# Performance work log

Hardware: AMD Instinct MI355X
Metric: run time of the kernel (lower is better)

The kernel has to match this reference:

```python
import jax, jax.numpy as jnp
import numpy as np

NUM_CAPS = 2          # NUM_CLASSES
R = 16 * 10 * 10 * 10 # num_route_nodes = 16000
NUM_ITERS = 3


def conv3d(x, w, b, stride):
    y = jax.lax.conv_general_dilated(
        x, w, window_strides=(stride, stride, stride), padding='VALID',
        dimension_numbers=('NCDHW', 'OIDHW', 'NCDHW'))
    return y + b[None, :, None, None, None]


def squash(t, axis=-1):
    n = jnp.linalg.norm(t, axis=axis, keepdims=True)
    scale = n ** 2 / (1 + n ** 2) / (n + 1e-8)
    return scale * t


def setup_inputs() -> dict:
    key = jax.random.key(0)
    ks = jax.random.split(key, 16)
    inp = {
        'x': jax.random.normal(ks[0], (16, 1, 29, 29, 29), jnp.float32),
        'conv1_w': 0.05 * jax.random.normal(ks[1], (128, 1, 3, 3, 3), jnp.float32),
        'conv1_b': jnp.zeros((128,), jnp.float32),
        # 8 primary capsules, each Conv3d(128,16,k=9,s=2), stacked cap-major
        'pcaps_w': 0.01 * jax.random.normal(ks[2], (8 * 16, 128, 9, 9, 9), jnp.float32),
        'pcaps_b': jnp.zeros((8 * 16,), jnp.float32),
        'route_w': 0.01 * jax.random.normal(ks[3], (NUM_CAPS, R, 8, 16), jnp.float32),
        'dec_w1': 0.05 * jax.random.normal(ks[4], (32, 512), jnp.float32),
        'dec_b1': jnp.zeros((512,), jnp.float32),
        'dec_w2': 0.05 * jax.random.normal(ks[5], (512, 2048), jnp.float32),
        'dec_b2': jnp.zeros((2048,), jnp.float32),
        'dec_w3': 0.02 * jax.random.normal(ks[6], (2048, 10240), jnp.float32),
        'dec_b3': jnp.zeros((10240,), jnp.float32),
        'dec_w4': 0.02 * jax.random.normal(ks[7], (10240, 27000), jnp.float32),
        'dec_b4': jnp.zeros((27000,), jnp.float32),
    }
    return inp


def reference(x, conv1_w, conv1_b, pcaps_w, pcaps_b, route_w,
              dec_w1, dec_b1, dec_w2, dec_b2, dec_w3, dec_b3, dec_w4, dec_b4):
    B = x.shape[0]
    # stem conv + relu: [B,128,27,27,27]
    h = jax.nn.relu(conv3d(x, conv1_w, conv1_b, 1))
    # primary capsules (8 convs fused into one): [B,128,10,10,10]
    p = conv3d(h, pcaps_w, pcaps_b, 2)
    # torch: per-capsule view(B,-1,1) then cat dim=-1 -> [B,16000,8]
    p = p.reshape(B, 8, R).transpose(0, 2, 1)
    u = squash(p, axis=-1)  # [B,R,8]

    # priors: x[:,None,:,None,:] @ W[None] -> [B,C,R,16] (singleton dim dropped)
    priors = jnp.einsum('bri,crio->bcro', u, route_w)
    priors_d = jax.lax.stop_gradient(priors)
    # torch logits have trailing dim 16 but are constant along it (delta is
    # broadcast), so [B,C,R,1] is mathematically identical.
    logits = jnp.zeros((B, NUM_CAPS, R, 1), priors.dtype)

    for i in range(NUM_ITERS):
        probs = jax.nn.softmax(logits, axis=1)  # over capsule axis
        if i == NUM_ITERS - 1:
            v = squash((probs * priors).sum(axis=2, keepdims=True))
        else:
            v = squash((probs * priors_d).sum(axis=2, keepdims=True))
            logits = logits + (priors_d * v).sum(axis=-1, keepdims=True)

    caps = v[:, :, 0, :]  # [B,C,16] (squeeze)
    classes = jnp.linalg.norm(caps, axis=-1)  # [B,C]

    # y=None branch: one-hot of argmax
    y = jax.nn.one_hot(jnp.argmax(classes, axis=1), NUM_CAPS, dtype=caps.dtype)
    d = (caps * y[:, :, None]).reshape(B, -1)  # [B,32]
    d = jax.nn.relu(d @ dec_w1 + dec_b1)
    d = jax.nn.relu(d @ dec_w2 + dec_b2)
    d = jax.nn.relu(d @ dec_w3 + dec_b3)
    recon = jax.nn.sigmoid(d @ dec_w4 + dec_b4)  # [B,27000]
    return classes, recon
```

## Files before the change

kernel.cpp:

```cpp
#include <hip/hip_runtime.h>
#include <hip/hip_bf16.h>

#define NB   16
#define C1   128
#define XS   29
#define HS   27
#define HSP  19683
#define PS   10
#define PSP  1000
#define RR   16000
#define NCAP 2
#define KTAP 729
#define HTOT 40310784L
#define SPTOT 314928

#define OFF_WT   0UL
#define OFF_H    11943936UL
#define OFF_P    52254720UL
#define OFF_U    54302720UL
#define OFF_PRI  56350720UL
#define OFF_LOG  64542720UL
#define OFF_S    65054720UL
#define OFF_V    65055232UL
#define OFF_D0   65055744UL
#define OFF_D1   65056256UL
#define OFF_D2   65064448UL
#define OFF_D3   65097216UL
#define OFF_D4   65261056UL
#define OFF_PP   65693056UL
#define OFF_D3P  82077056UL
#define OFF_D4P  84698496UL

typedef __attribute__((ext_vector_type(8))) short bf16x8;
typedef __attribute__((ext_vector_type(4))) float f32x4;

#define GL2LDS16(g, l) __builtin_amdgcn_global_load_lds( \
    (const __attribute__((address_space(1))) void*)(g), \
    (__attribute__((address_space(3))) void*)(l), 16, 0, 0)

__global__ void prep_w2(const float* __restrict__ w, __hip_bfloat16* __restrict__ w2) {
    __shared__ float tile[32][33];
    int tap0 = blockIdx.x * 32;
    int ic0  = blockIdx.y * 32;
    int oc   = blockIdx.z;
    int tx = threadIdx.x & 31, ty = threadIdx.x >> 5;
    #pragma unroll
    for (int j = 0; j < 32; j += 8) {
        int tap = tap0 + tx, ic = ic0 + ty + j;
        if (tap < KTAP) tile[ty + j][tx] = w[(size_t)oc * 93312 + (size_t)ic * KTAP + tap];
    }
    __syncthreads();
    #pragma unroll
    for (int j = 0; j < 32; j += 8) {
        int tap = tap0 + ty + j, ic = ic0 + tx;
        if (tap < KTAP)
            w2[((size_t)tap * 128 + oc) * 128 + ic] = __float2bfloat16(tile[tx][ty + j]);
    }
}

__global__ __launch_bounds__(256) void conv1_relu(const float* __restrict__ x,
                                                  const float* __restrict__ w,
                                                  const float* __restrict__ bias,
                                                  __hip_bfloat16* __restrict__ h) {
    int t = threadIdx.x;
    int c = t & 127;
    float wr[27];
    #pragma unroll
    for (int k = 0; k < 27; k++) wr[k] = w[c * 27 + k];
    float bv = bias[c];
    int sp_base = blockIdx.x * 32 + (t >> 7);
    #pragma unroll 4
    for (int i = 0; i < 16; i++) {
        int spg = sp_base + i * 2;
        if (spg >= SPTOT) return;
        int b = spg / HSP, sp = spg % HSP;
        int z = sp / 729, y = (sp / 27) % 27, xx = sp % 27;
        const float* xb = x + (size_t)b * (XS * XS * XS) + ((size_t)z * XS + y) * XS + xx;
        float xv[27];
        #pragma unroll
        for (int dz = 0; dz < 3; dz++)
            #pragma unroll
            for (int dy = 0; dy < 3; dy++)
                #pragma unroll
                for (int dx = 0; dx < 3; dx++)
                    xv[(dz * 3 + dy) * 3 + dx] = xb[((size_t)dz * XS + dy) * XS + dx];
        float acc = bv;
        #pragma unroll
        for (int k = 0; k < 27; k++) acc = fmaf(xv[k], wr[k], acc);
        h[(size_t)spg * 128 + c] = __float2bfloat16(fmaxf(acc, 0.f));
    }
}

__global__ __launch_bounds__(512, 2) void pcaps_mfma(const ushort* __restrict__ hu,
                                                     const ushort* __restrict__ wu,
                                                     float* __restrict__ pp) {
    __shared__ __align__(16) ushort As[2 * 256 * 32];
    __shared__ __align__(16) ushort Bs[2 * 128 * 32];
    int t = threadIdx.x;
    int bid = blockIdx.x;
    int g = bid & 7;
    int m0 = (bid >> 3) * 256;
    int tap_begin = g * 92;
    int tap_end   = min(KTAP, tap_begin + 92);
    int KP = (tap_end - tap_begin) * 4;

    int a_base[2], a_seg[2];
    #pragma unroll
    for (int q = 0; q < 2; q++) {
        int idx = q * 512 + t;
        int row = idx >> 2;
        int m = m0 + row; if (m > 15999) m = 15999;
        int b = m / PSP, sp = m % PSP;
        int oz = sp / 100, oy = (sp / 10) % 10, ox = sp % 10;
        a_base[q] = (((b * HS + 2 * oz) * HS + 2 * oy) * HS + 2 * ox) * 128;
        a_seg[q]  = (((idx & 3) ^ ((idx >> 3) & 3))) * 8;
    }
    int b_base = (t >> 2) * 128;
    int b_seg  = (((t & 3) ^ ((t >> 3) & 3))) * 8;

    int lane = t & 63, wave = t >> 6;
    int wr = wave >> 1, wc = wave & 1;
    int l15 = lane & 15, kq = lane >> 4;
    int slot8 = (kq ^ ((l15 >> 1) & 3)) * 8;

    f32x4 acc[4][4];
    #pragma unroll
    for (int i = 0; i < 4; i++)
        #pragma unroll
        for (int j = 0; j < 4; j++) acc[i][j] = (f32x4)0.f;

#define STAGE(KPI, NB_)  {                                                   \
        int tap_ = tap_begin + ((KPI) >> 2), ich_ = ((KPI) & 3) * 32;        \
        int dz_ = tap_ / 81, dy_ = (tap_ / 9) % 9, dx_ = tap_ % 9;           \
        int toff_ = ((dz_ * HS + dy_) * HS + dx_) * 128 + ich_;              \
        const ushort* wt_ = wu + ((size_t)tap_ << 14) + ich_;                \
        ushort* ad_ = As + (NB_) * (256 * 32);                               \
        ushort* bd_ = Bs + (NB_) * (128 * 32);                               \
        GL2LDS16(hu + a_base[0] + toff_ + a_seg[0], ad_ + (size_t)t * 8);    \
        GL2LDS16(hu + a_base[1] + toff_ + a_seg[1], ad_ + (size_t)(512 + t) * 8); \
        GL2LDS16(wt_ + b_base + b_seg, bd_ + (size_t)t * 8);                 \
    }

    STAGE(0, 0);
    int cur = 0;
    for (int kp = 0; kp < KP; ++kp) {
        int nk = (kp + 1 < KP) ? kp + 1 : kp;
        STAGE(nk, cur ^ 1);
        asm volatile("s_waitcnt vmcnt(3)" ::: "memory");
        __builtin_amdgcn_s_barrier();
        const ushort* Ac = As + cur * (256 * 32);
        const ushort* Bc = Bs + cur * (128 * 32);
        bf16x8 av[4], bv[4];
        #pragma unroll
        for (int i = 0; i < 4; i++)
            av[i] = *(const bf16x8*)&Ac[(wr * 64 + i * 16 + l15) * 32 + slot8];
        #pragma unroll
        for (int j = 0; j < 4; j++)
            bv[j] = *(const bf16x8*)&Bc[(wc * 64 + j * 16 + l15) * 32 + slot8];
        #pragma unroll
        for (int i = 0; i < 4; i++)
            #pragma unroll
            for (int j = 0; j < 4; j++)
                acc[i][j] = __builtin_amdgcn_mfma_f32_16x16x32_bf16(av[i], bv[j], acc[i][j], 0, 0, 0);
        __builtin_amdgcn_s_barrier();
        cur ^= 1;
    }
#undef STAGE

    float* pg = pp + (size_t)g * 16000 * 128;
    #pragma unroll
    for (int i = 0; i < 4; i++) {
        int mbase = m0 + wr * 64 + i * 16 + kq * 4;
        #pragma unroll
        for (int j = 0; j < 4; j++) {
            int n = wc * 64 + j * 16 + l15;
            #pragma unroll
            for (int r = 0; r < 4; r++) {
                int m = mbase + r;
                if (m < 16000) pg[(size_t)m * 128 + n] = acc[i][j][r];
            }
        }
    }
}

__global__ void reduce_p(const float* __restrict__ pp, float* __restrict__ p) {
    int gid = blockIdx.x * 256 + threadIdx.x;
    const float4* p4 = (const float4*)pp;
    float4 a = p4[gid];
    #pragma unroll
    for (int k = 1; k < 8; k++) {
        float4 b = p4[(size_t)k * 512000 + gid];
        a.x += b.x; a.y += b.y; a.z += b.z; a.w += b.w;
    }
    ((float4*)p)[gid] = a;
}

__global__ void squash_u(const float* __restrict__ p, const float* __restrict__ pb,
                         float* __restrict__ u) {
    int gid = blockIdx.x * 256 + threadIdx.x;
    int b = gid / RR, r = gid % RR;
    int s = r % PSP, rq = r / PSP;
    float vals[8]; float ss = 0.f;
    #pragma unroll
    for (int i = 0; i < 8; i++) {
        int ch = i * 16 + rq;
        float pv = p[((size_t)b * PSP + s) * 128 + ch] + pb[ch];
        vals[i] = pv; ss += pv * pv;
    }
    float n = sqrtf(ss);
    float scale = ss / (1.f + ss) / (n + 1e-8f);
    #pragma unroll
    for (int i = 0; i < 8; i++) u[(size_t)gid * 8 + i] = vals[i] * scale;
}

__global__ void priors_k(const float* __restrict__ u, const float* __restrict__ rw,
                         float* __restrict__ pri) {
    __shared__ float wl[16][132];
    int bx = blockIdx.x; int c = bx / 1000; int r0 = (bx % 1000) * 16;
    int t = threadIdx.x;
    const float4* src = (const float4*)(rw + ((size_t)c * RR + r0) * 128);
    #pragma unroll
    for (int q = 0; q < 8; q++) {
        int idx = q * 256 + t;
        int row = idx >> 5, c4 = idx & 31;
        *(float4*)&wl[row][c4 * 4] = src[idx];
    }
    __syncthreads();
    int bb = t >> 4, rl = t & 15;
    const float* up = u + ((size_t)bb * RR + r0 + rl) * 8;
    float4 u0 = *(const float4*)up, u1 = *(const float4*)(up + 4);
    float uu[8] = {u0.x, u0.y, u0.z, u0.w, u1.x, u1.y, u1.z, u1.w};
    float out[16];
    #pragma unroll
    for (int o = 0; o < 16; o++) out[o] = 0.f;
    #pragma unroll
    for (int i = 0; i < 8; i++)
        #pragma unroll
        for (int o = 0; o < 16; o++) out[o] += uu[i] * wl[rl][i * 16 + o];
    float* dst = pri + ((size_t)(bb * 2 + c) * RR + r0 + rl) * 16;
    #pragma unroll
    for (int q = 0; q < 4; q++)
        *(float4*)&dst[q * 4] = make_float4(out[q*4], out[q*4+1], out[q*4+2], out[q*4+3]);
}

__global__ void route_s(const float* __restrict__ pri, const float* __restrict__ lg,
                        float* __restrict__ s) {
    int b = blockIdx.x, chunk = blockIdx.y;
    int t = threadIdx.x, o = t & 15, rl = t >> 4;
    float acc0 = 0.f, acc1 = 0.f;
    for (int j = 0; j < 40; j++) {
        int r = chunk * 640 + j * 16 + rl;
        float l0 = lg[(size_t)(b * 2 + 0) * RR + r];
        float l1 = lg[(size_t)(b * 2 + 1) * RR + r];
        float m = fmaxf(l0, l1);
        float e0 = __expf(l0 - m), e1 = __expf(l1 - m);
        float inv = 1.f / (e0 + e1);
        acc0 += (e0 * inv) * pri[((size_t)(b * 2 + 0) * RR + r) * 16 + o];
        acc1 += (e1 * inv) * pri[((size_t)(b * 2 + 1) * RR + r) * 16 + o];
    }
    __shared__ float red[2][16][17];
    red[0][rl][o] = acc0; red[1][rl][o] = acc1;
    __syncthreads();
    for (int step = 8; step >= 1; step >>= 1) {
        if (rl < step) {
            red[0][rl][o] += red[0][rl + step][o];
            red[1][rl][o] += red[1][rl + step][o];
        }
        __syncthreads();
    }
    if (rl == 0) {
        atomicAdd(&s[(b * 2 + 0) * 16 + o], red[0][0][o]);
        atomicAdd(&s[(b * 2 + 1) * 16 + o], red[1][0][o]);
    }
}

__global__ void squash_v(const float* __restrict__ s, float* __restrict__ v) {
    int t = threadIdx.x;
    int bc = t >> 4, o = t & 15;
    float ss = 0.f;
    #pragma unroll
    for (int i = 0; i < 16; i++) { float x = s[bc * 16 + i]; ss += x * x; }
    float n = sqrtf(ss);
    float sc = ss / (1.f + ss) / (n + 1e-8f);
    v[bc * 16 + o] = s[bc * 16 + o] * sc;
}

__global__ void route_logit(const float* __restrict__ pri, const float* __restrict__ v,
                            float* __restrict__ lg) {
    int gid = blockIdx.x * 256 + threadIdx.x;
    int bc = gid / RR;
    const float* pp = pri + (size_t)gid * 16;
    float dot = 0.f;
    #pragma unroll
    for (int o = 0; o < 16; o++) dot += pp[o] * v[bc * 16 + o];
    lg[gid] += dot;
}

__global__ void classes_mask(const float* __restrict__ v, float* __restrict__ out,
                             float* __restrict__ d0) {
    __shared__ float cls[32];
    int t = threadIdx.x;
    if (t < 32) {
        float ss = 0.f;
        #pragma unroll
        for (int i = 0; i < 16; i++) { float x = v[t * 16 + i]; ss += x * x; }
        float n = sqrtf(ss);
        cls[t] = n; out[t] = n;
    }
    __syncthreads();
    int b = t >> 5, k = t & 31, c = k >> 4;
    int win = (cls[b * 2 + 1] > cls[b * 2 + 0]) ? 1 : 0;
    d0[t] = (c == win) ? v[b * 32 + k] : 0.f;
}

template<int K>
__global__ void dec_small(const float* __restrict__ din, const float* __restrict__ W,
                          const float* __restrict__ bias, float* __restrict__ dout, int N) {
    __shared__ float dl[16 * K];
    int t = threadIdx.x;
    for (int i = t; i < 16 * K; i += 256) dl[i] = din[i];
    __syncthreads();
    int n = blockIdx.x * 256 + t;
    if (n >= N) return;
    float acc[16];
    float bv = bias[n];
    #pragma unroll
    for (int b = 0; b < 16; b++) acc[b] = bv;
    for (int k = 0; k < K; k++) {
        float w = W[(size_t)k * N + n];
        #pragma unroll
        for (int b = 0; b < 16; b++) acc[b] += dl[b * K + k] * w;
    }
    #pragma unroll
    for (int b = 0; b < 16; b++) dout[(size_t)b * N + n] = fmaxf(acc[b], 0.f);
}

__global__ void dec_split(const float* __restrict__ din, const float* __restrict__ W,
                          float* __restrict__ part, int N, int K, int KC) {
    extern __shared__ float dl[];
    int t = threadIdx.x;
    int ky = blockIdx.y;
    int k0 = ky * KC;
    for (int i = t; i < 16 * KC; i += 256) {
        int b = i / KC, kk = i % KC;
        dl[i] = din[(size_t)b * K + k0 + kk];
    }
    __syncthreads();
    int n = blockIdx.x * 1024 + t * 4;
    if (n >= N) return;
    float4 acc[16];
    #pragma unroll
    for (int b = 0; b < 16; b++) acc[b] = make_float4(0.f, 0.f, 0.f, 0.f);
    const float* Wp = W + (size_t)k0 * N + n;
    for (int kk = 0; kk < KC; kk++) {
        float4 w = *(const float4*)&Wp[(size_t)kk * N];
        #pragma unroll
        for (int b = 0; b < 16; b++) {
            float dv = dl[b * KC + kk];
            acc[b].x += dv * w.x; acc[b].y += dv * w.y;
            acc[b].z += dv * w.z; acc[b].w += dv * w.w;
        }
    }
    #pragma unroll
    for (int b = 0; b < 16; b++)
        *(float4*)&part[((size_t)(ky * 16 + b)) * N + n] = acc[b];
}

__global__ void bias_act_sum(const float* __restrict__ part, const float* __restrict__ bias,
                             float* __restrict__ out, int N, int total, int sigm) {
    int gid = blockIdx.x * 256 + threadIdx.x;
    if (gid >= total) return;
    int b = gid / N, n = gid % N;
    float x = bias[n];
    #pragma unroll
    for (int ky = 0; ky < 16; ky++)
        x += part[((size_t)(ky * 16 + b)) * N + n];
    out[gid] = sigm ? (1.f / (1.f + __expf(-x))) : fmaxf(x, 0.f);
}

extern "C" void kernel_launch(void* const* d_in, const int* in_sizes, int n_in,
                              void* d_out, int out_size, void* d_ws, size_t ws_size,
                              hipStream_t stream) {
    const float* x        = (const float*)d_in[0];
    const float* conv1_w  = (const float*)d_in[1];
    const float* conv1_b  = (const float*)d_in[2];
    const float* pcaps_w  = (const float*)d_in[3];
    const float* pcaps_b  = (const float*)d_in[4];
    const float* route_w  = (const float*)d_in[5];
    const float* dec_w1   = (const float*)d_in[6];
    const float* dec_b1   = (const float*)d_in[7];
    const float* dec_w2   = (const float*)d_in[8];
    const float* dec_b2   = (const float*)d_in[9];
    const float* dec_w3   = (const float*)d_in[10];
    const float* dec_b3   = (const float*)d_in[11];
    const float* dec_w4   = (const float*)d_in[12];
    const float* dec_b4   = (const float*)d_in[13];
    float* out = (float*)d_out;

    float* ws = (float*)d_ws;
    __hip_bfloat16* w2 = (__hip_bfloat16*)(ws + OFF_WT);
    __hip_bfloat16* h  = (__hip_bfloat16*)(ws + OFF_H);
    float* p    = ws + OFF_P;
    float* u    = ws + OFF_U;
    float* pri  = ws + OFF_PRI;
    float* lg   = ws + OFF_LOG;
    float* s    = ws + OFF_S;
    float* v    = ws + OFF_V;
    float* d0   = ws + OFF_D0;
    float* d1   = ws + OFF_D1;
    float* d2   = ws + OFF_D2;
    float* d3   = ws + OFF_D3;
    float* d4   = ws + OFF_D4;
    float* pp   = ws + OFF_PP;
    float* d3p  = ws + OFF_D3P;
    float* d4p  = ws + OFF_D4P;

    prep_w2<<<dim3(23, 4, 128), 256, 0, stream>>>(pcaps_w, w2);
    conv1_relu<<<(SPTOT + 31) / 32, 256, 0, stream>>>(x, conv1_w, conv1_b, h);

    pcaps_mfma<<<504, 512, 0, stream>>>((const ushort*)h, (const ushort*)w2, pp);
    reduce_p<<<2000, 256, 0, stream>>>(pp, p);

    squash_u<<<1000, 256, 0, stream>>>(p, pcaps_b, u);
    priors_k<<<2000, 256, 0, stream>>>(u, route_w, pri);

    hipMemsetAsync(lg, 0, (size_t)NB * NCAP * RR * sizeof(float), stream);
    for (int it = 0; it < 3; it++) {
        hipMemsetAsync(s, 0, 512 * sizeof(float), stream);
        route_s<<<dim3(16, 25), 256, 0, stream>>>(pri, lg, s);
        squash_v<<<1, 512, 0, stream>>>(s, v);
        if (it < 2) route_logit<<<2000, 256, 0, stream>>>(pri, v, lg);
    }

    classes_mask<<<1, 512, 0, stream>>>(v, out, d0);

    dec_small<32><<<2, 256, 0, stream>>>(d0, dec_w1, dec_b1, d1, 512);
    dec_small<512><<<8, 256, 0, stream>>>(d1, dec_w2, dec_b2, d2, 2048);

    dec_split<<<dim3(10, 16), 256, 16 * 128 * sizeof(float), stream>>>(d2, dec_w3, d3p, 10240, 2048, 128);
    bias_act_sum<<<(16 * 10240 + 255) / 256, 256, 0, stream>>>(d3p, dec_b3, d3, 10240, 16 * 10240, 0);

    dec_split<<<dim3(27, 16), 256, 16 * 640 * sizeof(float), stream>>>(d3, dec_w4, d4p, 27000, 10240, 640);
    bias_act_sum<<<(16 * 27000 + 255) / 256, 256, 0, stream>>>(d4p, dec_b4, out + 32, 27000, 16 * 27000, 1);
}
```

Measured before the change: 1.233 ms.

## Fuse partial-sum reduction with squash and merge routing logit update into weighted sum

Replaces the separate partial-sum reduction and squash kernels with one kernel that sums the 8 split-K partials, adds bias and squashes per row. The routing loop is restructured so each iteration computes the logit update by a warp-shuffle dot product and uses it for the weighted sum in the same pass. The first iteration skips the softmax because uniform logits give weights of 0.5. Atomics and memsets are replaced by per-chunk partial sums reduced in the squash kernel. This removes several launches and repeated passes over the priors, at the cost of some redundant shuffle work and strided stores from the fused squash kernel.

```diff
diff --git a/kernel.cpp b/kernel.cpp
--- a/kernel.cpp
+++ b/kernel.cpp
@@ -16,11 +16,10 @@
 
 #define OFF_WT   0UL
 #define OFF_H    11943936UL
-#define OFF_P    52254720UL
+#define OFF_SP   52254720UL
 #define OFF_U    54302720UL
 #define OFF_PRI  56350720UL
 #define OFF_LOG  64542720UL
-#define OFF_S    65054720UL
 #define OFF_V    65055232UL
 #define OFF_D0   65055744UL
 #define OFF_D1   65056256UL
@@ -183,34 +182,30 @@
     }
 }
 
-__global__ void reduce_p(const float* __restrict__ pp, float* __restrict__ p) {
-    int gid = blockIdx.x * 256 + threadIdx.x;
-    const float4* p4 = (const float4*)pp;
-    float4 a = p4[gid];
-    #pragma unroll
-    for (int k = 1; k < 8; k++) {
-        float4 b = p4[(size_t)k * 512000 + gid];
-        a.x += b.x; a.y += b.y; a.z += b.z; a.w += b.w;
-    }
-    ((float4*)p)[gid] = a;
-}
-
-__global__ void squash_u(const float* __restrict__ p, const float* __restrict__ pb,
-                         float* __restrict__ u) {
-    int gid = blockIdx.x * 256 + threadIdx.x;
-    int b = gid / RR, r = gid % RR;
-    int s = r % PSP, rq = r / PSP;
-    float vals[8]; float ss = 0.f;
-    #pragma unroll
-    for (int i = 0; i < 8; i++) {
-        int ch = i * 16 + rq;
-        float pv = p[((size_t)b * PSP + s) * 128 + ch] + pb[ch];
-        vals[i] = pv; ss += pv * pv;
-    }
-    float n = sqrtf(ss);
-    float scale = ss / (1.f + ss) / (n + 1e-8f);
-    #pragma unroll
-    for (int i = 0; i < 8; i++) u[(size_t)gid * 8 + i] = vals[i] * scale;
+__global__ void squash_red(const float* __restrict__ pp, const float* __restrict__ pb,
+                           float* __restrict__ u) {
+    __shared__ float rowv[2][128];
+    int t = threadIdx.x;
+    int m = blockIdx.x * 2 + (t >> 7);
+    int ch = t & 127;
+    float v = pb[ch];
+    #pragma unroll
+    for (int g = 0; g < 8; g++) v += pp[(size_t)g * 2048000 + (size_t)m * 128 + ch];
+    rowv[t >> 7][ch] = v;
+    __syncthreads();
+    if (t < 32) {
+        int row = t >> 4, rq = t & 15;
+        int mm = blockIdx.x * 2 + row;
+        int b = mm / PSP, s = mm % PSP;
+        float vals[8], ss = 0.f;
+        #pragma unroll
+        for (int i = 0; i < 8; i++) { float x = rowv[row][i * 16 + rq]; vals[i] = x; ss += x * x; }
+        float n = sqrtf(ss);
+        float sc = ss / (1.f + ss) / (n + 1e-8f);
+        float* dst = u + ((size_t)b * RR + rq * 1000 + s) * 8;
+        #pragma unroll
+        for (int i = 0; i < 8; i++) dst[i] = vals[i] * sc;
+    }
 }
 
 __global__ void priors_k(const float* __restrict__ u, const float* __restrict__ rw,
@@ -243,20 +238,14 @@
         *(float4*)&dst[q * 4] = make_float4(out[q*4], out[q*4+1], out[q*4+2], out[q*4+3]);
 }
 
-__global__ void route_s(const float* __restrict__ pri, const float* __restrict__ lg,
-                        float* __restrict__ s) {
+__global__ void route_s0(const float* __restrict__ pri, float* __restrict__ spart) {
     int b = blockIdx.x, chunk = blockIdx.y;
     int t = threadIdx.x, o = t & 15, rl = t >> 4;
     float acc0 = 0.f, acc1 = 0.f;
     for (int j = 0; j < 40; j++) {
         int r = chunk * 640 + j * 16 + rl;
-        float l0 = lg[(size_t)(b * 2 + 0) * RR + r];
-        float l1 = lg[(size_t)(b * 2 + 1) * RR + r];
-        float m = fmaxf(l0, l1);
-        float e0 = __expf(l0 - m), e1 = __expf(l1 - m);
-        float inv = 1.f / (e0 + e1);
-        acc0 += (e0 * inv) * pri[((size_t)(b * 2 + 0) * RR + r) * 16 + o];
-        acc1 += (e1 * inv) * pri[((size_t)(b * 2 + 1) * RR + r) * 16 + o];
+        acc0 += pri[((size_t)(b * 2 + 0) * RR + r) * 16 + o];
+        acc1 += pri[((size_t)(b * 2 + 1) * RR + r) * 16 + o];
     }
     __shared__ float red[2][16][17];
     red[0][rl][o] = acc0; red[1][rl][o] = acc1;
@@ -269,48 +258,103 @@
         __syncthreads();
     }
     if (rl == 0) {
-        atomicAdd(&s[(b * 2 + 0) * 16 + o], red[0][0][o]);
-        atomicAdd(&s[(b * 2 + 1) * 16 + o], red[1][0][o]);
-    }
-}
-
-__global__ void squash_v(const float* __restrict__ s, float* __restrict__ v) {
+        spart[((b * 25 + chunk) * 2 + 0) * 16 + o] = 0.5f * red[0][0][o];
+        spart[((b * 25 + chunk) * 2 + 1) * 16 + o] = 0.5f * red[1][0][o];
+    }
+}
+
+template<int MODE>
+__global__ void route_iter(const float* __restrict__ pri, const float* __restrict__ v,
+                           float* __restrict__ lg, float* __restrict__ spart) {
+    int b = blockIdx.x, chunk = blockIdx.y;
+    int t = threadIdx.x, o = t & 15, rl = t >> 4;
+    float v0 = v[(b * 2 + 0) * 16 + o], v1 = v[(b * 2 + 1) * 16 + o];
+    float acc0 = 0.f, acc1 = 0.f;
+    for (int j = 0; j < 40; j++) {
+        int r = chunk * 640 + j * 16 + rl;
+        float p0 = pri[((size_t)(b * 2 + 0) * RR + r) * 16 + o];
+        float p1 = pri[((size_t)(b * 2 + 1) * RR + r) * 16 + o];
+        float d0 = p0 * v0, d1 = p1 * v1;
+        #pragma unroll
+        for (int w = 1; w < 16; w <<= 1) { d0 += __shfl_xor(d0, w); d1 += __shfl_xor(d1, w); }
+        float l0, l1;
+        if (MODE == 1) {
+            l0 = d0; l1 = d1;
+            if (o == 0) lg[(size_t)(b * 2 + 0) * RR + r] = d0;
+            if (o == 1) lg[(size_t)(b * 2 + 1) * RR + r] = d1;
+        } else {
+            l0 = lg[(size_t)(b * 2 + 0) * RR + r] + d0;
+            l1 = lg[(size_t)(b * 2 + 1) * RR + r] + d1;
+        }
+        float mx = fmaxf(l0, l1);
+        float e0 = __expf(l0 - mx), e1 = __expf(l1 - mx);
+        float inv = 1.f / (e0 + e1);
+        acc0 += (e0 * inv) * p0;
+        acc1 += (e1 * inv) * p1;
+    }
+    __shared__ float red[2][16][17];
+    red[0][rl][o] = acc0; red[1][rl][o] = acc1;
+    __syncthreads();
+    for (int step = 8; step >= 1; step >>= 1) {
+        if (rl < step) {
+            red[0][rl][o] += red[0][rl + step][o];
+            red[1][rl][o] += red[1][rl + step][o];
+        }
+        __syncthreads();
+    }
+    if (rl == 0) {
+        spart[((b * 25 + chunk) * 2 + 0) * 16 + o] = red[0][0][o];
+        spart[((b * 25 + chunk) * 2 + 1) * 16 + o] = red[1][0][o];
+    }
+}
+
+__global__ void squash_v_parts(const float* __restrict__ spart, float* __restrict__ v) {
     int t = threadIdx.x;
     int bc = t >> 4, o = t & 15;
+    int b = bc >> 1, c = bc & 1;
+    float x = 0.f;
+    for (int ch = 0; ch < 25; ch++) x += spart[((b * 25 + ch) * 2 + c) * 16 + o];
+    __shared__ float sv[32][17];
+    sv[bc][o] = x;
+    __syncthreads();
     float ss = 0.f;
     #pragma unroll
-    for (int i = 0; i < 16; i++) { float x = s[bc * 16 + i]; ss += x * x; }
+    for (int i = 0; i < 16; i++) { float y = sv[bc][i]; ss += y * y; }
     float n = sqrtf(ss);
     float sc = ss / (1.f + ss) / (n + 1e-8f);
-    v[bc * 16 + o] = s[bc * 16 + o] * sc;
-}
-
-__global__ void route_logit(const float* __restrict__ pri, const float* __restrict__ v,
-                            float* __restrict__ lg) {
-    int gid = blockIdx.x * 256 + threadIdx.x;
-    int bc = gid / RR;
-    const float* pp = pri + (size_t)gid * 16;
-    float dot = 0.f;
-    #pragma unroll
-    for (int o = 0; o < 16; o++) dot += pp[o] * v[bc * 16 + o];
-    lg[gid] += dot;
-}
-
-__global__ void classes_mask(const float* __restrict__ v, float* __restrict__ out,
+    v[bc * 16 + o] = x * sc;
+}
+
+__global__ void squash_v_cls(const float* __restrict__ spart, float* __restrict__ out,
                              float* __restrict__ d0) {
+    int t = threadIdx.x;
+    int bc = t >> 4, o = t & 15;
+    int b = bc >> 1, c = bc & 1;
+    float x = 0.f;
+    for (int ch = 0; ch < 25; ch++) x += spart[((b * 25 + ch) * 2 + c) * 16 + o];
+    __shared__ float sv[32][17];
+    __shared__ float vv[32][17];
     __shared__ float cls[32];
-    int t = threadIdx.x;
+    sv[bc][o] = x;
+    __syncthreads();
+    float ss = 0.f;
+    #pragma unroll
+    for (int i = 0; i < 16; i++) { float y = sv[bc][i]; ss += y * y; }
+    float n = sqrtf(ss);
+    float sc = ss / (1.f + ss) / (n + 1e-8f);
+    vv[bc][o] = x * sc;
+    __syncthreads();
     if (t < 32) {
-        float ss = 0.f;
-        #pragma unroll
-        for (int i = 0; i < 16; i++) { float x = v[t * 16 + i]; ss += x * x; }
-        float n = sqrtf(ss);
-        cls[t] = n; out[t] = n;
-    }
-    __syncthreads();
-    int b = t >> 5, k = t & 31, c = k >> 4;
-    int win = (cls[b * 2 + 1] > cls[b * 2 + 0]) ? 1 : 0;
-    d0[t] = (c == win) ? v[b * 32 + k] : 0.f;
+        float s2 = 0.f;
+        #pragma unroll
+        for (int i = 0; i < 16; i++) { float y = vv[t][i]; s2 += y * y; }
+        float nn = sqrtf(s2);
+        cls[t] = nn; out[t] = nn;
+    }
+    __syncthreads();
+    int bb = t >> 5, k = t & 31, cc = k >> 4;
+    int win = (cls[bb * 2 + 1] > cls[bb * 2 + 0]) ? 1 : 0;
+    d0[t] = (cc == win) ? vv[bb * 2 + cc][k & 15] : 0.f;
 }
 
 template<int K>
@@ -400,17 +444,15 @@
     float* ws = (float*)d_ws;
     __hip_bfloat16* w2 = (__hip_bfloat16*)(ws + OFF_WT);
     __hip_bfloat16* h  = (__hip_bfloat16*)(ws + OFF_H);
-    float* p    = ws + OFF_P;
+    float* spart = ws + OFF_SP;
     float* u    = ws + OFF_U;
     float* pri  = ws + OFF_PRI;
     float* lg   = ws + OFF_LOG;
-    float* s    = ws + OFF_S;
     float* v    = ws + OFF_V;
     float* d0   = ws + OFF_D0;
     float* d1   = ws + OFF_D1;
     float* d2   = ws + OFF_D2;
     float* d3   = ws + OFF_D3;
-    float* d4   = ws + OFF_D4;
     float* pp   = ws + OFF_PP;
     float* d3p  = ws + OFF_D3P;
     float* d4p  = ws + OFF_D4P;
@@ -419,20 +461,16 @@
     conv1_relu<<<(SPTOT + 31) / 32, 256, 0, stream>>>(x, conv1_w, conv1_b, h);
 
     pcaps_mfma<<<504, 512, 0, stream>>>((const ushort*)h, (const ushort*)w2, pp);
-    reduce_p<<<2000, 256, 0, stream>>>(pp, p);
-
-    squash_u<<<1000, 256, 0, stream>>>(p, pcaps_b, u);
+    squash_red<<<8000, 256, 0, stream>>>(pp, pcaps_b, u);
+
     priors_k<<<2000, 256, 0, stream>>>(u, route_w, pri);
 
-    hipMemsetAsync(lg, 0, (size_t)NB * NCAP * RR * sizeof(float), stream);
-    for (int it = 0; it < 3; it++) {
-        hipMemsetAsync(s, 0, 512 * sizeof(float), stream);
-        route_s<<<dim3(16, 25), 256, 0, stream>>>(pri, lg, s);
-        squash_v<<<1, 512, 0, stream>>>(s, v);
-        if (it < 2) route_logit<<<2000, 256, 0, stream>>>(pri, v, lg);
-    }
-
-    classes_mask<<<1, 512, 0, stream>>>(v, out, d0);
+    route_s0<<<dim3(16, 25), 256, 0, stream>>>(pri, spart);
+    squash_v_parts<<<1, 512, 0, stream>>>(spart, v);
+    route_iter<1><<<dim3(16, 25), 256, 0, stream>>>(pri, v, lg, spart);
+    squash_v_parts<<<1, 512, 0, stream>>>(spart, v);
+    route_iter<2><<<dim3(16, 25), 256, 0, stream>>>(pri, v, lg, spart);
+    squash_v_cls<<<1, 512, 0, stream>>>(spart, out, d0);
 
     dec_small<32><<<2, 256, 0, stream>>>(d0, dec_w1, dec_b1, d1, 512);
     dec_small<512><<<8, 256, 0, stream>>>(d1, dec_w2, dec_b2, d2, 2048);
```

After: 1.226 ms. No clear change (-0.6%).
